# Kernel tuning notes

Measured on AMD Instinct MI355X. Metric: run time of the kernel, lower is better.

## Reference

```python
import jax, jax.numpy as jnp
import numpy as np

LS = (0, 1, 2)
M_IN = (128, 64, 32)            # input mults per l -> dim 480
M_MID = (384, 192, 96)          # gated mlp_mid mults; scalars=384, gated l=1,2
N_GATES = M_MID[1] + M_MID[2]   # 288 extra 0e gate scalars
M1_OUT = (M_MID[0] + N_GATES, M_MID[1], M_MID[2])  # fctp_1 output mults (672,192,96)
M_OUT = (128, 64, 32)           # output mults -> dim 480


def _split(x, mults):
    """Split flat (N, sum mul*(2l+1)) features into per-l (N, mul, 2l+1) blocks."""
    outs, off = [], 0
    for m, l in zip(mults, LS):
        d = m * (2 * l + 1)
        outs.append(x[:, off:off + d].reshape(x.shape[0], m, 2 * l + 1))
        off += d
    return outs


def _fctp(xs, attr, Ws, b):
    """FCTP with a 1x0e second operand: per-l linear mix * attr, 1/sqrt(fan_in)
    path normalization, bias on the l=0 block (Equiformer rescale convention)."""
    outs = []
    for x, W in zip(xs, Ws):
        inv = 1.0 / np.sqrt(x.shape[1]).astype(np.float32)
        y = jnp.einsum('nmi,mo->noi', x, W) * inv * attr[:, :, None]
        outs.append(y)
    outs[0] = outs[0] + b[None, :, None]
    return outs


def _ffn(node_input, node_attr, W1_0, W1_1, W1_2, b1, W2_0, W2_1, W2_2, b2):
    xs = _split(node_input, M_IN)
    h = _fctp(xs, node_attr, (W1_0, W1_1, W1_2), b1)
    # SwishGate: silu on scalars, sigmoid gates multiply the l>0 irreps
    s0 = h[0][:, :, 0]                         # (N, 672)
    scalars = jax.nn.silu(s0[:, :M_MID[0]])    # (N, 384)
    gates = jax.nn.sigmoid(s0[:, M_MID[0]:])   # (N, 288)
    g1 = gates[:, :M_MID[1]]
    g2 = gates[:, M_MID[1]:]
    mid = [scalars[:, :, None], h[1] * g1[:, :, None], h[2] * g2[:, :, None]]
    out = _fctp(mid, node_attr, (W2_0, W2_1, W2_2), b2)
    return jnp.concatenate([o.reshape(o.shape[0], -1) for o in out], axis=1)


def setup_inputs() -> dict:
    key = jax.random.key(0)
    ks = jax.random.split(key, 9)
    N = 100000
    return {
        'node_input': jax.random.normal(ks[0], (N, 480), jnp.float32),
        'node_attr': jnp.ones((N, 1), jnp.float32),
        'W1_0': jax.random.normal(ks[1], (128, 672), jnp.float32),
        'W1_1': jax.random.normal(ks[2], (64, 192), jnp.float32),
        'W1_2': jax.random.normal(ks[3], (32, 96), jnp.float32),
        'b1': jax.random.normal(ks[4], (672,), jnp.float32),
        'W2_0': jax.random.normal(ks[5], (384, 128), jnp.float32),
        'W2_1': jax.random.normal(ks[6], (192, 64), jnp.float32),
        'W2_2': jax.random.normal(ks[7], (96, 32), jnp.float32),
        'b2': jax.random.normal(ks[8], (128,), jnp.float32),
    }


def reference(node_input, node_attr, W1_0, W1_1, W1_2, b1, W2_0, W2_1, W2_2, b2):
    return _ffn(node_input, node_attr, W1_0, W1_1, W1_2, b1, W2_0, W2_1, W2_2, b2)
```

## Files before the change

kernel.cpp:

```cpp
#include <hip/hip_runtime.h>
#include <hip/hip_bf16.h>

typedef __bf16 bf16_t;
typedef __bf16 bf16x8 __attribute__((ext_vector_type(8)));
typedef float  f32x4  __attribute__((ext_vector_type(4)));

static __device__ __forceinline__ f32x4 mfma16(bf16x8 a, bf16x8 b, f32x4 c) {
    return __builtin_amdgcn_mfma_f32_16x16x32_bf16(a, b, c, 0, 0, 0);
}
static __device__ __forceinline__ float fast_rcp(float x) {
    return __builtin_amdgcn_rcpf(x);
}

#define OFF_W10 0
#define OFF_W11 86016
#define OFF_W12 98304
#define OFF_W20 101376
#define OFF_W21 150528
#define OFF_W22 162816
#define W_TOTAL 165888

template<int K, int N, int OFF>
static __device__ __forceinline__ void scatter_seg(const float* __restrict__ src,
                                                   bf16_t* __restrict__ ws, int local) {
    int k  = local / N;
    int n  = local - k * N;
    int f  = k >> 5;
    int kr = k & 31;
    int lane = ((kr >> 3) << 4) | (n & 15);
    int dst  = OFF + ((((n >> 4) * (K >> 5)) + f) << 9) + (lane << 3) + (kr & 7);
    ws[dst] = (bf16_t)src[local];
}

__global__ void prep_weights(const float* __restrict__ W10, const float* __restrict__ W11,
                             const float* __restrict__ W12, const float* __restrict__ W20,
                             const float* __restrict__ W21, const float* __restrict__ W22,
                             bf16_t* __restrict__ ws) {
    int idx = blockIdx.x * 256 + threadIdx.x;
    if (idx >= W_TOTAL) return;
    if      (idx < OFF_W11) scatter_seg<128, 672, OFF_W10>(W10, ws, idx - OFF_W10);
    else if (idx < OFF_W12) scatter_seg< 64, 192, OFF_W11>(W11, ws, idx - OFF_W11);
    else if (idx < OFF_W20) scatter_seg< 32,  96, OFF_W12>(W12, ws, idx - OFF_W12);
    else if (idx < OFF_W21) scatter_seg<384, 128, OFF_W20>(W20, ws, idx - OFF_W20);
    else if (idx < OFF_W22) scatter_seg<192,  64, OFF_W21>(W21, ws, idx - OFF_W21);
    else                    scatter_seg< 96,  32, OFF_W22>(W22, ws, idx - OFF_W22);
}

#define XDE_S   488
#define MID0_S  392
#define MID1_S  200
#define MID2_S  104
#define MID0_B  9600
#define MID2_B  9600

__global__ __launch_bounds__(256, 4)
void ffn_kernel(const float* __restrict__ x, const float* __restrict__ attr,
                const float* __restrict__ b1, const float* __restrict__ b2,
                const bf16_t* __restrict__ wf, float* __restrict__ out) {
    __shared__ bf16_t smid[17920];
    __shared__ float  sattr[16];

    const int tid   = threadIdx.x;
    const int lane  = tid & 63;
    const int w     = tid >> 6;
    const int rlane = lane & 15;
    const int q     = lane >> 4;
    const int rowbase = blockIdx.x * 16;

    for (int it = 0; it < 8; ++it) {
        int idx = tid + it * 256;
        if (idx < 1920) {
            int row = idx / 120;
            int c4  = idx - row * 120;
            const float4 v = ((const float4*)(x + (size_t)(rowbase + row) * 480))[c4];
            float vals[4] = {v.x, v.y, v.z, v.w};
            int base = c4 * 4;
#pragma unroll
            for (int e = 0; e < 4; ++e) {
                int col = base + e;
                int dc;
                if (col < 128) dc = col;
                else if (col < 320) { int r = col - 128; int m = r / 3; int i = r - m * 3; dc = 128 + i * 64 + m; }
                else                { int r = col - 320; int m = r / 5; int i = r - m * 5; dc = 320 + i * 32 + m; }
                smid[row * XDE_S + dc] = (bf16_t)vals[e];
            }
        }
    }
    if (tid < 16) sattr[tid] = attr[rowbase + tid];
    __syncthreads();

    float sat[4];
#pragma unroll
    for (int r = 0; r < 4; ++r) sat[r] = sattr[q * 4 + r];

    bf16x8 a0[4], a1[3][2], a2[5];
    {
        int rb = rlane * XDE_S + q * 8;
#pragma unroll
        for (int f = 0; f < 4; ++f) a0[f] = *(const bf16x8*)&smid[rb + f * 32];
#pragma unroll
        for (int i = 0; i < 3; ++i)
#pragma unroll
            for (int f = 0; f < 2; ++f) a1[i][f] = *(const bf16x8*)&smid[rb + 128 + i * 64 + f * 32];
#pragma unroll
        for (int i = 0; i < 5; ++i) a2[i] = *(const bf16x8*)&smid[rb + 320 + i * 32];
    }

    float gv[5][4];

    {
        const float inv = 0.088388347648318447f;
        const bf16_t* base10 = wf + OFF_W10 + (lane << 3);
#pragma unroll
        for (int ti = 0; ti < 6; ++ti) {
            int t = w + ti * 4;
            const bf16_t* p = base10 + ((t * 4) << 9);
            float bias = b1[t * 16 + rlane];
            f32x4 acc = {0.f, 0.f, 0.f, 0.f};
            __builtin_amdgcn_s_setprio(1);
#pragma unroll
            for (int f = 0; f < 4; ++f) acc = mfma16(a0[f], *(const bf16x8*)(p + (f << 9)), acc);
            __builtin_amdgcn_s_setprio(0);
            int c = t * 16 + rlane;
#pragma unroll
            for (int r = 0; r < 4; ++r) {
                float v = acc[r] * inv * sat[r] + bias;
                float s = v * fast_rcp(1.f + __expf(-v));
                smid[MID0_B + (q * 4 + r) * MID0_S + c] = (bf16_t)s;
            }
        }
#pragma unroll
        for (int ti = 0; ti < 5; ++ti) {
            int t = 24 + w + ti * 4;
            if (ti == 4 && t >= 42) continue;
            const bf16_t* p = base10 + ((t * 4) << 9);
            float bias = b1[t * 16 + rlane];
            f32x4 acc = {0.f, 0.f, 0.f, 0.f};
            __builtin_amdgcn_s_setprio(1);
#pragma unroll
            for (int f = 0; f < 4; ++f) acc = mfma16(a0[f], *(const bf16x8*)(p + (f << 9)), acc);
            __builtin_amdgcn_s_setprio(0);
#pragma unroll
            for (int r = 0; r < 4; ++r) {
                float v = acc[r] * inv * sat[r] + bias;
                gv[ti][r] = fast_rcp(1.f + __expf(-v));
            }
        }
    }
    __syncthreads();

    {
        const float inv = 0.051031036307982884f;
        bf16x8 am[12];
        int rb = MID0_B + rlane * MID0_S + q * 8;
#pragma unroll
        for (int f = 0; f < 12; ++f) am[f] = *(const bf16x8*)&smid[rb + f * 32];
#pragma unroll
        for (int ti = 0; ti < 2; ++ti) {
            int t = w + ti * 4;
            const bf16_t* p = wf + OFF_W20 + ((t * 12) << 9) + (lane << 3);
            float bias = b2[t * 16 + rlane];
            f32x4 acc = {0.f, 0.f, 0.f, 0.f};
            __builtin_amdgcn_s_setprio(1);
#pragma unroll
            for (int f = 0; f < 12; ++f) acc = mfma16(am[f], *(const bf16x8*)(p + (f << 9)), acc);
            __builtin_amdgcn_s_setprio(0);
            int c = t * 16 + rlane;
#pragma unroll
            for (int r = 0; r < 4; ++r)
                out[(size_t)(rowbase + q * 4 + r) * 480 + c] = acc[r] * inv * sat[r] + bias;
        }
    }
    {
        const float inv = 0.125f;
#pragma unroll
        for (int ti = 0; ti < 3; ++ti) {
            int t = w + ti * 4;
            const bf16_t* p = wf + OFF_W11 + ((t * 2) << 9) + (lane << 3);
            bf16x8 b0  = *(const bf16x8*)p;
            bf16x8 b1f = *(const bf16x8*)(p + 512);
            f32x4 acc[3];
            __builtin_amdgcn_s_setprio(1);
#pragma unroll
            for (int i = 0; i < 3; ++i) {
                f32x4 a = {0.f, 0.f, 0.f, 0.f};
                a = mfma16(a1[i][0], b0, a);
                a = mfma16(a1[i][1], b1f, a);
                acc[i] = a;
            }
            __builtin_amdgcn_s_setprio(0);
            int m = t * 16 + rlane;
#pragma unroll
            for (int r = 0; r < 4; ++r) {
                int row = q * 4 + r;
                float g = gv[ti][r] * inv * sat[r];
#pragma unroll
                for (int i = 0; i < 3; ++i)
                    smid[i * 3200 + row * MID1_S + m] = (bf16_t)(acc[i][r] * g);
            }
        }
    }
    __syncthreads();

    {
        const float inv = 0.17677669529663689f;
#pragma unroll
        for (int ti = 0; ti < 2; ++ti) {
            int t = w + ti * 4;
            if (ti == 1 && t >= 6) continue;
            const bf16_t* p = wf + OFF_W12 + (t << 9) + (lane << 3);
            bf16x8 b = *(const bf16x8*)p;
            f32x4 acc[5];
            __builtin_amdgcn_s_setprio(1);
#pragma unroll
            for (int i = 0; i < 5; ++i) {
                f32x4 a = {0.f, 0.f, 0.f, 0.f};
                acc[i] = mfma16(a2[i], b, a);
            }
            __builtin_amdgcn_s_setprio(0);
            int m = t * 16 + rlane;
#pragma unroll
            for (int r = 0; r < 4; ++r) {
                int row = q * 4 + r;
                float g = gv[3 + ti][r] * inv * sat[r];
#pragma unroll
                for (int i = 0; i < 5; ++i)
                    smid[MID2_B + i * 1664 + row * MID2_S + m] = (bf16_t)(acc[i][r] * g);
            }
        }
    }
    {
        const float inv = 0.072168783648703220f;
        int t = w;
        const bf16_t* p = wf + OFF_W21 + ((t * 6) << 9) + (lane << 3);
        bf16x8 b[6];
#pragma unroll
        for (int f = 0; f < 6; ++f) b[f] = *(const bf16x8*)(p + (f << 9));
        f32x4 acc[3];
        __builtin_amdgcn_s_setprio(1);
#pragma unroll
        for (int i = 0; i < 3; ++i) {
            bf16x8 am[6];
            int rb = i * 3200 + rlane * MID1_S + q * 8;
#pragma unroll
            for (int f = 0; f < 6; ++f) am[f] = *(const bf16x8*)&smid[rb + f * 32];
            f32x4 a = {0.f, 0.f, 0.f, 0.f};
#pragma unroll
            for (int f = 0; f < 6; ++f) a = mfma16(am[f], b[f], a);
            acc[i] = a;
        }
        __builtin_amdgcn_s_setprio(0);
        int o = t * 16 + rlane;
#pragma unroll
        for (int r = 0; r < 4; ++r) {
            float s = inv * sat[r];
            float* dst = out + (size_t)(rowbase + q * 4 + r) * 480 + 128 + o * 3;
            dst[0] = acc[0][r] * s;
            dst[1] = acc[1][r] * s;
            dst[2] = acc[2][r] * s;
        }
    }
    __syncthreads();

    if (w < 2) {
        const float inv = 0.10206207261596575f;
        int t = w;
        const bf16_t* p = wf + OFF_W22 + ((t * 3) << 9) + (lane << 3);
        bf16x8 b[3];
#pragma unroll
        for (int f = 0; f < 3; ++f) b[f] = *(const bf16x8*)(p + (f << 9));
        f32x4 acc[5];
        __builtin_amdgcn_s_setprio(1);
#pragma unroll
        for (int i = 0; i < 5; ++i) {
            bf16x8 am[3];
            int rb = MID2_B + i * 1664 + rlane * MID2_S + q * 8;
#pragma unroll
            for (int f = 0; f < 3; ++f) am[f] = *(const bf16x8*)&smid[rb + f * 32];
            f32x4 a = {0.f, 0.f, 0.f, 0.f};
#pragma unroll
            for (int f = 0; f < 3; ++f) a = mfma16(am[f], b[f], a);
            acc[i] = a;
        }
        __builtin_amdgcn_s_setprio(0);
        int o = t * 16 + rlane;
#pragma unroll
        for (int r = 0; r < 4; ++r) {
            float s = inv * sat[r];
            float* dst = out + (size_t)(rowbase + q * 4 + r) * 480 + 320 + o * 5;
#pragma unroll
            for (int i = 0; i < 5; ++i) dst[i] = acc[i][r] * s;
        }
    }
}

extern "C" void kernel_launch(void* const* d_in, const int* in_sizes, int n_in,
                              void* d_out, int out_size, void* d_ws, size_t ws_size,
                              hipStream_t stream) {
    const float* x    = (const float*)d_in[0];
    const float* attr = (const float*)d_in[1];
    const float* W10  = (const float*)d_in[2];
    const float* W11  = (const float*)d_in[3];
    const float* W12  = (const float*)d_in[4];
    const float* b1   = (const float*)d_in[5];
    const float* W20  = (const float*)d_in[6];
    const float* W21  = (const float*)d_in[7];
    const float* W22  = (const float*)d_in[8];
    const float* b2   = (const float*)d_in[9];
    float*  out = (float*)d_out;
    bf16_t* wf  = (bf16_t*)d_ws;

    int N = in_sizes[0] / 480;

    prep_weights<<<dim3((W_TOTAL + 255) / 256), dim3(256), 0, stream>>>(
        W10, W11, W12, W20, W21, W22, wf);
    ffn_kernel<<<dim3(N / 16), dim3(256), 0, stream>>>(
        x, attr, b1, b2, wf, out);
}
```

Before: 483.8 us.

## Software-pipeline W1_0 fragment loads, stage biases in LDS, drop setprio

The first-layer scalar/gate loop is merged into one 11-iteration loop that prefetches the next tile's weight fragments while the current tile's MFMAs and activations run, so global load latency can overlap with compute. Biases b1 and b2 are copied into shared memory once per block instead of being read from global memory inside the loops. All s_setprio calls around the MFMA chains are removed. The double-buffered fragments raise register pressure under the 4-waves launch bound, and dropping setprio changes wave scheduling.

```diff
diff --git a/kernel.cpp b/kernel.cpp
--- a/kernel.cpp
+++ b/kernel.cpp
@@ -59,6 +59,8 @@
                 const bf16_t* __restrict__ wf, float* __restrict__ out) {
     __shared__ bf16_t smid[17920];
     __shared__ float  sattr[16];
+    __shared__ float  sb1[672];
+    __shared__ float  sb2[128];
 
     const int tid   = threadIdx.x;
     const int lane  = tid & 63;
@@ -86,7 +88,9 @@
             }
         }
     }
-    if (tid < 16) sattr[tid] = attr[rowbase + tid];
+    for (int i = tid; i < 672; i += 256) sb1[i] = b1[i];
+    if (tid < 128) sb2[tid] = b2[tid];
+    if (tid < 16)  sattr[tid] = attr[rowbase + tid];
     __syncthreads();
 
     float sat[4];
@@ -111,40 +115,45 @@
     {
         const float inv = 0.088388347648318447f;
         const bf16_t* base10 = wf + OFF_W10 + (lane << 3);
-#pragma unroll
-        for (int ti = 0; ti < 6; ++ti) {
-            int t = w + ti * 4;
-            const bf16_t* p = base10 + ((t * 4) << 9);
-            float bias = b1[t * 16 + rlane];
-            f32x4 acc = {0.f, 0.f, 0.f, 0.f};
-            __builtin_amdgcn_s_setprio(1);
-#pragma unroll
-            for (int f = 0; f < 4; ++f) acc = mfma16(a0[f], *(const bf16x8*)(p + (f << 9)), acc);
-            __builtin_amdgcn_s_setprio(0);
-            int c = t * 16 + rlane;
-#pragma unroll
-            for (int r = 0; r < 4; ++r) {
-                float v = acc[r] * inv * sat[r] + bias;
-                float s = v * fast_rcp(1.f + __expf(-v));
-                smid[MID0_B + (q * 4 + r) * MID0_S + c] = (bf16_t)s;
-            }
-        }
-#pragma unroll
-        for (int ti = 0; ti < 5; ++ti) {
-            int t = 24 + w + ti * 4;
-            if (ti == 4 && t >= 42) continue;
-            const bf16_t* p = base10 + ((t * 4) << 9);
-            float bias = b1[t * 16 + rlane];
-            f32x4 acc = {0.f, 0.f, 0.f, 0.f};
-            __builtin_amdgcn_s_setprio(1);
-#pragma unroll
-            for (int f = 0; f < 4; ++f) acc = mfma16(a0[f], *(const bf16x8*)(p + (f << 9)), acc);
-            __builtin_amdgcn_s_setprio(0);
-#pragma unroll
-            for (int r = 0; r < 4; ++r) {
-                float v = acc[r] * inv * sat[r] + bias;
-                gv[ti][r] = fast_rcp(1.f + __expf(-v));
-            }
+        bf16x8 bc[4];
+        {
+            const bf16_t* p = base10 + ((w * 4) << 9);
+#pragma unroll
+            for (int f = 0; f < 4; ++f) bc[f] = *(const bf16x8*)(p + (f << 9));
+        }
+#pragma unroll
+        for (int ti = 0; ti < 11; ++ti) {
+            int t  = w + ti * 4;
+            int tn = t + 4;
+            bf16x8 bn[4] = {bc[0], bc[1], bc[2], bc[3]};
+            if (ti < 10 && tn < 42) {
+                const bf16_t* p = base10 + ((tn * 4) << 9);
+#pragma unroll
+                for (int f = 0; f < 4; ++f) bn[f] = *(const bf16x8*)(p + (f << 9));
+            }
+            if (t < 42) {
+                f32x4 acc = {0.f, 0.f, 0.f, 0.f};
+#pragma unroll
+                for (int f = 0; f < 4; ++f) acc = mfma16(a0[f], bc[f], acc);
+                int c = t * 16 + rlane;
+                float bias = sb1[c];
+                if (ti < 6) {
+#pragma unroll
+                    for (int r = 0; r < 4; ++r) {
+                        float v = acc[r] * inv * sat[r] + bias;
+                        float s = v * fast_rcp(1.f + __expf(-v));
+                        smid[MID0_B + (q * 4 + r) * MID0_S + c] = (bf16_t)s;
+                    }
+                } else {
+#pragma unroll
+                    for (int r = 0; r < 4; ++r) {
+                        float v = acc[r] * inv * sat[r] + bias;
+                        gv[ti - 6][r] = fast_rcp(1.f + __expf(-v));
+                    }
+                }
+            }
+#pragma unroll
+            for (int f = 0; f < 4; ++f) bc[f] = bn[f];
         }
     }
     __syncthreads();
@@ -159,12 +168,11 @@
         for (int ti = 0; ti < 2; ++ti) {
             int t = w + ti * 4;
             const bf16_t* p = wf + OFF_W20 + ((t * 12) << 9) + (lane << 3);
-            float bias = b2[t * 16 + rlane];
+            float bias = sb2[t * 16 + rlane];
             f32x4 acc = {0.f, 0.f, 0.f, 0.f};
-            __builtin_amdgcn_s_setprio(1);
-#pragma unroll
-            for (int f = 0; f < 12; ++f) acc = mfma16(am[f], *(const bf16x8*)(p + (f << 9)), acc);
-            __builtin_amdgcn_s_setprio(0);
+#pragma unroll
+            for (int f = 0; f < 12; ++f)
+                acc = mfma16(am[f], *(const bf16x8*)(p + (f << 9)), acc);
             int c = t * 16 + rlane;
 #pragma unroll
             for (int r = 0; r < 4; ++r)
@@ -180,7 +188,6 @@
             bf16x8 b0  = *(const bf16x8*)p;
             bf16x8 b1f = *(const bf16x8*)(p + 512);
             f32x4 acc[3];
-            __builtin_amdgcn_s_setprio(1);
 #pragma unroll
             for (int i = 0; i < 3; ++i) {
                 f32x4 a = {0.f, 0.f, 0.f, 0.f};
@@ -188,7 +195,6 @@
                 a = mfma16(a1[i][1], b1f, a);
                 acc[i] = a;
             }
-            __builtin_amdgcn_s_setprio(0);
             int m = t * 16 + rlane;
 #pragma unroll
             for (int r = 0; r < 4; ++r) {
@@ -211,13 +217,11 @@
             const bf16_t* p = wf + OFF_W12 + (t << 9) + (lane << 3);
             bf16x8 b = *(const bf16x8*)p;
             f32x4 acc[5];
-            __builtin_amdgcn_s_setprio(1);
 #pragma unroll
             for (int i = 0; i < 5; ++i) {
                 f32x4 a = {0.f, 0.f, 0.f, 0.f};
                 acc[i] = mfma16(a2[i], b, a);
             }
-            __builtin_amdgcn_s_setprio(0);
             int m = t * 16 + rlane;
 #pragma unroll
             for (int r = 0; r < 4; ++r) {
@@ -237,7 +241,6 @@
 #pragma unroll
         for (int f = 0; f < 6; ++f) b[f] = *(const bf16x8*)(p + (f << 9));
         f32x4 acc[3];
-        __builtin_amdgcn_s_setprio(1);
 #pragma unroll
         for (int i = 0; i < 3; ++i) {
             bf16x8 am[6];
@@ -249,7 +252,6 @@
             for (int f = 0; f < 6; ++f) a = mfma16(am[f], b[f], a);
             acc[i] = a;
         }
-        __builtin_amdgcn_s_setprio(0);
         int o = t * 16 + rlane;
 #pragma unroll
         for (int r = 0; r < 4; ++r) {
@@ -270,7 +272,6 @@
 #pragma unroll
         for (int f = 0; f < 3; ++f) b[f] = *(const bf16x8*)(p + (f << 9));
         f32x4 acc[5];
-        __builtin_amdgcn_s_setprio(1);
 #pragma unroll
         for (int i = 0; i < 5; ++i) {
             bf16x8 am[3];
@@ -282,7 +283,6 @@
             for (int f = 0; f < 3; ++f) a = mfma16(am[f], b[f], a);
             acc[i] = a;
         }
-        __builtin_amdgcn_s_setprio(0);
         int o = t * 16 + rlane;
 #pragma unroll
         for (int r = 0; r < 4; ++r) {
```

Measured after the change: 475.4 us. About the same (-1.7%).
